# Performance work log

Hardware: AMD Instinct MI355X
Metric: run time of the kernel (lower is better)

## Reference

```python
import jax, jax.numpy as jnp
import numpy as np

N_NODES = 50000
N_EDGES = 800000
D_IN = 128
H1 = 128
H2 = 64
N_CLASSES = 4


def _sage_conv(x, src, dst, w_l, w_r, b, num_nodes):
    # PyG SAGEConv (aggr='mean'): out = lin_l(mean_{j->i} x_j) + lin_r(x_i)
    ones = jnp.ones((src.shape[0],), dtype=x.dtype)
    deg = jax.ops.segment_sum(ones, dst, num_segments=num_nodes)  # [N]
    agg = jax.ops.segment_sum(x[src], dst, num_segments=num_nodes)  # [N, d]
    agg = agg / jnp.maximum(deg, 1.0)[:, None]
    return agg @ w_l + b + x @ w_r


def setup_inputs() -> dict:
    key = jax.random.key(0)
    ks = jax.random.split(key, 12)
    x_content = jax.random.normal(ks[0], (N_NODES, D_IN), dtype=jnp.float32)
    edge_index = jax.random.randint(ks[1], (2, N_EDGES), 0, N_NODES, dtype=jnp.int32)
    edge_type = jax.random.randint(ks[2], (N_EDGES,), 0, 4, dtype=jnp.int32)
    s = 0.05
    params = {
        'w_l0': jax.random.normal(ks[3], (D_IN, H1), jnp.float32) * s,
        'w_r0': jax.random.normal(ks[4], (D_IN, H1), jnp.float32) * s,
        'b0': jnp.zeros((H1,), jnp.float32),
        'w_l1': jax.random.normal(ks[5], (H1, H1), jnp.float32) * s,
        'w_r1': jax.random.normal(ks[6], (H1, H1), jnp.float32) * s,
        'b1': jnp.zeros((H1,), jnp.float32),
        'w_l2': jax.random.normal(ks[7], (H1, H2), jnp.float32) * s,
        'w_r2': jax.random.normal(ks[8], (H1, H2), jnp.float32) * s,
        'b2': jnp.zeros((H2,), jnp.float32),
        'w_out': jax.random.normal(ks[9], (H2, N_CLASSES), jnp.float32) * s,
        'b_out': jnp.zeros((N_CLASSES,), jnp.float32),
    }
    return {'x_content': x_content, 'edge_index': edge_index, 'edge_type': edge_type, **params}


def reference(x_content, edge_index, edge_type,
              w_l0, w_r0, b0, w_l1, w_r1, b1, w_l2, w_r2, b2, w_out, b_out):
    # eval mode: dropout is identity
    src, dst = edge_index[0], edge_index[1]
    n = x_content.shape[0]
    x = x_content
    for (wl, wr, b) in ((w_l0, w_r0, b0), (w_l1, w_r1, b1), (w_l2, w_r2, b2)):
        x = _sage_conv(x, src, dst, wl, wr, b, n)
        x = jax.nn.relu(x)
    return x @ w_out + b_out
```

## Files before the change

kernel.cpp:

```cpp
#include <hip/hip_runtime.h>
#include <hip/hip_fp16.h>

#define D 128

constexpr int RSH = 14;
constexpr int RSZ = 1 << RSH;
constexpr int NRANGE = 4;
constexpr int CSH = 15;
constexpr int CSZ = 1 << CSH;

using short8 = __attribute__((ext_vector_type(8))) short;
using f32x4 = __attribute__((ext_vector_type(4))) float;

__device__ inline void splitf(float v, unsigned short& h, unsigned short& l) {
    unsigned b = __float_as_uint(v);
    h = (unsigned short)(b >> 16);
    float fh = __uint_as_float(b & 0xffff0000u);
    float r = v - fh;
    l = (unsigned short)(__float_as_uint(r) >> 16);
}

struct WSplitArgs {
    const float* src[6];
    unsigned short* dh[6];
    unsigned short* dl[6];
    int n[6];
};

__global__ __launch_bounds__(256) void split_w(WSplitArgs a) {
    int m = blockIdx.y;
    int N = a.n[m];
    int e = blockIdx.x * 256 + threadIdx.x;
    if (e >= 128 * N) return;
    int sh = (N == 128) ? 7 : 6;
    int k = e >> sh;
    int n = e & (N - 1);
    float v = a.src[m][e];
    unsigned short h, l;
    splitf(v, h, l);
    a.dh[m][n * 128 + k] = h;
    a.dl[m][n * 128 + k] = l;
}

__global__ __launch_bounds__(1024) void hist_gemm_x(
    const int* __restrict__ dst, unsigned* __restrict__ hist,
    unsigned short* __restrict__ rank, int n_edges, int nchunk, int nhist,
    const float* __restrict__ X,
    const unsigned short* __restrict__ W1h, const unsigned short* __restrict__ W1l,
    const unsigned short* __restrict__ W2h, const unsigned short* __restrict__ W2l,
    const float* __restrict__ bias, __half* __restrict__ P, float* __restrict__ Q, int M) {
    __shared__ __align__(16) char smem[2 * 16 * 65 * 16];

    const int b = blockIdx.x;
    const int tid = threadIdx.x;

    if (b < nhist) {
        unsigned* lh = (unsigned*)smem;
        int r = b & (NRANGE - 1), c = b >> 2;
        for (int i = tid; i < RSZ / 2; i += 1024) lh[i] = 0;
        __syncthreads();
        int e0 = c << CSH, e1 = min(n_edges, e0 + CSZ);
        for (int e = e0 + tid; e < e1; e += 1024) {
            int d = dst[e];
            if ((d >> RSH) == r) {
                int ii = d & (RSZ - 1);
                unsigned sh = (ii & 1) * 16;
                unsigned old = atomicAdd(&lh[ii >> 1], 1u << sh);
                rank[e] = (unsigned short)((old >> sh) & 0xffffu);
            }
        }
        __syncthreads();
        unsigned* gh = hist + (size_t)(r * nchunk + c) * (RSZ / 2);
        for (int i = tid; i < RSZ / 2; i += 1024) gh[i] = lh[i];
        return;
    }

    short8(*As)[16 * 65] = (short8(*)[16 * 65])smem;
    const int wave = tid >> 6;
    const int lane = tid & 63;
    const int l15 = lane & 15;
    const int q = lane >> 4;
    const int m0 = (b - nhist) * 64;

    {
        int row = tid >> 4, col16 = tid & 15;
        int gr = min(m0 + row, M - 1);
        const float4* xp = (const float4*)X + (size_t)gr * 32 + col16 * 2;
        float4 v0 = xp[0], v1 = xp[1];
        float fv[8] = {v0.x, v0.y, v0.z, v0.w, v1.x, v1.y, v1.z, v1.w};
        short8 h, l;
#pragma unroll
        for (int j = 0; j < 8; ++j) {
            unsigned short hh_, ll_;
            splitf(fv[j], hh_, ll_);
            h[j] = (short)hh_;
            l[j] = (short)ll_;
        }
        As[0][col16 * 65 + row] = h;
        As[1][col16 * 65 + row] = l;
    }
    __syncthreads();

    const int isQ = wave >> 3;
    const int colbase = (wave & 7) * 16;
    const unsigned short* Wh = isQ ? W2h : W1h;
    const unsigned short* Wl = isQ ? W2l : W1l;
    const float bv = isQ ? bias[colbase + l15] : 0.f;
    const int wbase = (colbase + l15) * 128 + q * 8;

    f32x4 acc[4] = {};
    short8 Bh = *(const short8*)(Wh + wbase);
    short8 Bl = *(const short8*)(Wl + wbase);

#pragma unroll 1
    for (int kt = 0; kt < 4; ++kt) {
        short8 nBh, nBl;
        if (kt < 3) {
            nBh = *(const short8*)(Wh + wbase + (kt + 1) * 32);
            nBl = *(const short8*)(Wl + wbase + (kt + 1) * 32);
        }
#pragma unroll
        for (int mt = 0; mt < 4; ++mt) {
            int ai = (kt * 4 + q) * 65 + mt * 16 + l15;
            short8 Afh = As[0][ai];
            short8 Afl = As[1][ai];
            acc[mt] = __builtin_amdgcn_mfma_f32_16x16x32_bf16(Afh, Bh, acc[mt], 0, 0, 0);
            acc[mt] = __builtin_amdgcn_mfma_f32_16x16x32_bf16(Afh, Bl, acc[mt], 0, 0, 0);
            acc[mt] = __builtin_amdgcn_mfma_f32_16x16x32_bf16(Afl, Bh, acc[mt], 0, 0, 0);
        }
        Bh = nBh; Bl = nBl;
    }

    const int col = colbase + l15;
#pragma unroll
    for (int mt = 0; mt < 4; ++mt) {
        int orow = m0 + mt * 16 + q * 4;
#pragma unroll
        for (int r = 0; r < 4; ++r) {
            int rr = orow + r;
            if (rr < M) {
                if (isQ) Q[(size_t)rr * 128 + col] = acc[mt][r] + bv;
                else P[(size_t)rr * 128 + col] = __float2half(acc[mt][r]);
            }
        }
    }
}

__global__ __launch_bounds__(256) void deg_sum_partials(
    const unsigned short* __restrict__ hist16, int* __restrict__ deg,
    int* __restrict__ partials, int n_nodes, int nchunk) {
    __shared__ int sd[256];
    int b = blockIdx.x, t = threadIdx.x;
    int i = b * 256 + t;
    int s = 0;
    if (i < n_nodes) {
        int r = i >> RSH, ii = i & (RSZ - 1);
        const unsigned short* hp = hist16 + (size_t)r * nchunk * RSZ + ii;
        for (int c = 0; c < nchunk; ++c) s += hp[(size_t)c * RSZ];
        deg[i] = s;
    }
    sd[t] = s;
    __syncthreads();
    for (int st = 128; st > 0; st >>= 1) {
        if (t < st) sd[t] += sd[t + st];
        __syncthreads();
    }
    if (t == 0) partials[b] = sd[0];
}

__global__ __launch_bounds__(256) void scan_fill(
    const int* __restrict__ deg, const int* __restrict__ partials,
    const unsigned short* __restrict__ hist16, int* __restrict__ row_ptr,
    float* __restrict__ inv_deg, int* __restrict__ base,
    int n_nodes, int nchunk, int nblk) {
    __shared__ int sp[256];
    __shared__ int sd[256];
    int b = blockIdx.x, t = threadIdx.x;

    sp[t] = (t < b && t < nblk) ? partials[t] : 0;
    __syncthreads();
    for (int st = 128; st > 0; st >>= 1) {
        if (t < st) sp[t] += sp[t + st];
        __syncthreads();
    }
    int pbase = sp[0];

    int i = b * 256 + t;
    int v = (i < n_nodes) ? deg[i] : 0;
    sd[t] = v;
    __syncthreads();
    for (int d = 1; d < 256; d <<= 1) {
        int x = (t >= d) ? sd[t - d] : 0;
        __syncthreads();
        sd[t] += x;
        __syncthreads();
    }
    int excl = sd[t] - v + pbase;
    if (i < n_nodes) {
        row_ptr[i] = excl;
        int dv = v > 1 ? v : 1;
        inv_deg[i] = 1.0f / (float)dv;
        if (i == n_nodes - 1) row_ptr[n_nodes] = excl + v;
        int r = i >> RSH, ii = i & (RSZ - 1);
        int bacc = excl;
        for (int c = 0; c < nchunk; ++c) {
            size_t idx = (size_t)(r * nchunk + c) * RSZ + ii;
            base[idx] = bacc;
            bacc += hist16[idx];
        }
    }
}

__global__ __launch_bounds__(256) void fill_edges(
    const int* __restrict__ src, const int* __restrict__ dst,
    const unsigned short* __restrict__ rank, const int* __restrict__ base,
    int* __restrict__ csr, int n_edges, int nchunk) {
    int e = blockIdx.x * 256 + threadIdx.x;
    if (e >= n_edges) return;
    int d = dst[e];
    int c = e >> CSH;
    int r = d >> RSH;
    int slot = base[(size_t)(r * nchunk + c) * RSZ + (d & (RSZ - 1))] + rank[e];
    csr[slot] = src[e];
}

template <int BN>
__global__ __launch_bounds__(2 * (BN / 16) * 64) void gemm_wide(
    const unsigned short* __restrict__ Ah, const unsigned short* __restrict__ Al,
    const unsigned short* __restrict__ W1h, const unsigned short* __restrict__ W1l,
    const unsigned short* __restrict__ W2h, const unsigned short* __restrict__ W2l,
    const float* __restrict__ bias, __half* __restrict__ P, float* __restrict__ Q, int M) {
    __shared__ short8 As[2][16 * 65];
    constexpr int NW = BN / 16;
    constexpr int NTH = 2 * NW * 64;

    const int tid = threadIdx.x;
    const int wave = tid >> 6;
    const int lane = tid & 63;
    const int l15 = lane & 15;
    const int q = lane >> 4;
    const int m0 = blockIdx.x * 64;

#pragma unroll
    for (int it = 0; it < 2048 / NTH; ++it) {
        int s = it * NTH + tid;
        int arr = s >> 10;
        int sp = s & 1023;
        int row = sp >> 4, col16 = sp & 15;
        int gr = min(m0 + row, M - 1);
        const unsigned short* src = (arr ? Al : Ah) + (size_t)gr * 128 + col16 * 8;
        As[arr][col16 * 65 + row] = *(const short8*)src;
    }
    __syncthreads();

    const int isQ = wave >= NW;
    const int colbase = (isQ ? (wave - NW) : wave) * 16;
    const unsigned short* Wh = isQ ? W2h : W1h;
    const unsigned short* Wl = isQ ? W2l : W1l;
    const float bv = isQ ? bias[colbase + l15] : 0.f;
    const int wbase = (colbase + l15) * 128 + q * 8;

    f32x4 acc[4] = {};
    short8 Bh = *(const short8*)(Wh + wbase);
    short8 Bl = *(const short8*)(Wl + wbase);

#pragma unroll 1
    for (int kt = 0; kt < 4; ++kt) {
        short8 nBh, nBl;
        if (kt < 3) {
            nBh = *(const short8*)(Wh + wbase + (kt + 1) * 32);
            nBl = *(const short8*)(Wl + wbase + (kt + 1) * 32);
        }
#pragma unroll
        for (int mt = 0; mt < 4; ++mt) {
            int ai = (kt * 4 + q) * 65 + mt * 16 + l15;
            short8 Afh = As[0][ai];
            short8 Afl = As[1][ai];
            acc[mt] = __builtin_amdgcn_mfma_f32_16x16x32_bf16(Afh, Bh, acc[mt], 0, 0, 0);
            acc[mt] = __builtin_amdgcn_mfma_f32_16x16x32_bf16(Afh, Bl, acc[mt], 0, 0, 0);
            acc[mt] = __builtin_amdgcn_mfma_f32_16x16x32_bf16(Afl, Bh, acc[mt], 0, 0, 0);
        }
        Bh = nBh; Bl = nBl;
    }

    const int col = colbase + l15;
#pragma unroll
    for (int mt = 0; mt < 4; ++mt) {
        int orow = m0 + mt * 16 + q * 4;
#pragma unroll
        for (int r = 0; r < 4; ++r) {
            int rr = orow + r;
            if (rr < M) {
                if (isQ) Q[(size_t)rr * BN + col] = acc[mt][r] + bv;
                else P[(size_t)rr * BN + col] = __float2half(acc[mt][r]);
            }
        }
    }
}

__global__ __launch_bounds__(256) void agg_fused128(
    const __half* __restrict__ P, const float* __restrict__ Q,
    const int* __restrict__ row_ptr, const int* __restrict__ csr,
    const float* __restrict__ inv_deg, unsigned short* __restrict__ Hh,
    unsigned short* __restrict__ Hl, int n_nodes) {
    int node = (blockIdx.x * blockDim.x + threadIdx.x) >> 6;
    int lane = threadIdx.x & 63;
    if (node >= n_nodes) return;
    int beg = row_ptr[node], end = row_ptr[node + 1];
    const int g = lane >> 4;
    const int l = lane & 15;
    float a[4][8] = {};
    int e = beg;
    bool have = (e + 16 <= end);
    int i0 = 0, i1 = 0, i2 = 0, i3 = 0;
    if (have) { i0 = csr[e + g]; i1 = csr[e + 4 + g]; i2 = csr[e + 8 + g]; i3 = csr[e + 12 + g]; }
    while (have) {
        int en = e + 16;
        bool hn = (en + 16 <= end);
        int n0 = 0, n1 = 0, n2 = 0, n3 = 0;
        if (hn) { n0 = csr[en + g]; n1 = csr[en + 4 + g]; n2 = csr[en + 8 + g]; n3 = csr[en + 12 + g]; }
        int ss[4] = {i0, i1, i2, i3};
#pragma unroll
        for (int j = 0; j < 4; ++j) {
            uint4 raw = *(const uint4*)(P + (size_t)ss[j] * 128 + l * 8);
            float2 f01 = __half22float2(*reinterpret_cast<__half2*>(&raw.x));
            float2 f23 = __half22float2(*reinterpret_cast<__half2*>(&raw.y));
            float2 f45 = __half22float2(*reinterpret_cast<__half2*>(&raw.z));
            float2 f67 = __half22float2(*reinterpret_cast<__half2*>(&raw.w));
            a[j][0] += f01.x; a[j][1] += f01.y; a[j][2] += f23.x; a[j][3] += f23.y;
            a[j][4] += f45.x; a[j][5] += f45.y; a[j][6] += f67.x; a[j][7] += f67.y;
        }
        e = en; i0 = n0; i1 = n1; i2 = n2; i3 = n3; have = hn;
    }
    if (e < end) {
        int p0 = e + g, p1 = e + 4 + g, p2 = e + 8 + g, p3 = e + 12 + g;
        int j0 = (p0 < end) ? csr[p0] : -1;
        int j1 = (p1 < end) ? csr[p1] : -1;
        int j2 = (p2 < end) ? csr[p2] : -1;
        int j3 = (p3 < end) ? csr[p3] : -1;
        int ss[4] = {j0, j1, j2, j3};
#pragma unroll
        for (int j = 0; j < 4; ++j) {
            if (ss[j] >= 0) {
                uint4 raw = *(const uint4*)(P + (size_t)ss[j] * 128 + l * 8);
                float2 f01 = __half22float2(*reinterpret_cast<__half2*>(&raw.x));
                float2 f23 = __half22float2(*reinterpret_cast<__half2*>(&raw.y));
                float2 f45 = __half22float2(*reinterpret_cast<__half2*>(&raw.z));
                float2 f67 = __half22float2(*reinterpret_cast<__half2*>(&raw.w));
                a[j][0] += f01.x; a[j][1] += f01.y; a[j][2] += f23.x; a[j][3] += f23.y;
                a[j][4] += f45.x; a[j][5] += f45.y; a[j][6] += f67.x; a[j][7] += f67.y;
            }
        }
    }
    float s[8];
#pragma unroll
    for (int k = 0; k < 8; ++k) {
        s[k] = (a[0][k] + a[1][k]) + (a[2][k] + a[3][k]);
        s[k] += __shfl_xor(s[k], 16);
        s[k] += __shfl_xor(s[k], 32);
    }
    if (lane < 16) {
        float w = inv_deg[node];
        const float4* Q4 = (const float4*)Q;
        float4 q0 = Q4[(size_t)node * 32 + 2 * l];
        float4 q1 = Q4[(size_t)node * 32 + 2 * l + 1];
        float h0 = fmaxf(fmaf(s[0], w, q0.x), 0.f);
        float h1 = fmaxf(fmaf(s[1], w, q0.y), 0.f);
        float h2 = fmaxf(fmaf(s[2], w, q0.z), 0.f);
        float h3 = fmaxf(fmaf(s[3], w, q0.w), 0.f);
        float h4 = fmaxf(fmaf(s[4], w, q1.x), 0.f);
        float h5 = fmaxf(fmaf(s[5], w, q1.y), 0.f);
        float h6 = fmaxf(fmaf(s[6], w, q1.z), 0.f);
        float h7 = fmaxf(fmaf(s[7], w, q1.w), 0.f);
        ushort4 hv0, lv0, hv1, lv1;
        splitf(h0, hv0.x, lv0.x);
        splitf(h1, hv0.y, lv0.y);
        splitf(h2, hv0.z, lv0.z);
        splitf(h3, hv0.w, lv0.w);
        splitf(h4, hv1.x, lv1.x);
        splitf(h5, hv1.y, lv1.y);
        splitf(h6, hv1.z, lv1.z);
        splitf(h7, hv1.w, lv1.w);
        ((ushort4*)Hh)[(size_t)node * 32 + 2 * l] = hv0;
        ((ushort4*)Hh)[(size_t)node * 32 + 2 * l + 1] = hv1;
        ((ushort4*)Hl)[(size_t)node * 32 + 2 * l] = lv0;
        ((ushort4*)Hl)[(size_t)node * 32 + 2 * l + 1] = lv1;
    }
}

__global__ __launch_bounds__(256) void agg64_head(
    const __half* __restrict__ P, const float* __restrict__ Q,
    const int* __restrict__ row_ptr, const int* __restrict__ csr,
    const float* __restrict__ inv_deg, const float* __restrict__ Wo,
    const float* __restrict__ bo, float* __restrict__ out, int n_nodes) {
    int node = (blockIdx.x * blockDim.x + threadIdx.x) >> 6;
    int lane = threadIdx.x & 63;
    if (node >= n_nodes) return;
    int beg = row_ptr[node], end = row_ptr[node + 1];
    const int g = lane >> 4;
    const int l = lane & 15;
    float a[4][4] = {};
    int e = beg;
    bool have = (e + 16 <= end);
    int i0 = 0, i1 = 0, i2 = 0, i3 = 0;
    if (have) { i0 = csr[e + g]; i1 = csr[e + 4 + g]; i2 = csr[e + 8 + g]; i3 = csr[e + 12 + g]; }
    while (have) {
        int en = e + 16;
        bool hn = (en + 16 <= end);
        int n0 = 0, n1 = 0, n2 = 0, n3 = 0;
        if (hn) { n0 = csr[en + g]; n1 = csr[en + 4 + g]; n2 = csr[en + 8 + g]; n3 = csr[en + 12 + g]; }
        int ss[4] = {i0, i1, i2, i3};
#pragma unroll
        for (int j = 0; j < 4; ++j) {
            uint2 raw = *(const uint2*)(P + (size_t)ss[j] * 64 + l * 4);
            float2 f01 = __half22float2(*reinterpret_cast<__half2*>(&raw.x));
            float2 f23 = __half22float2(*reinterpret_cast<__half2*>(&raw.y));
            a[j][0] += f01.x; a[j][1] += f01.y; a[j][2] += f23.x; a[j][3] += f23.y;
        }
        e = en; i0 = n0; i1 = n1; i2 = n2; i3 = n3; have = hn;
    }
    if (e < end) {
        int p0 = e + g, p1 = e + 4 + g, p2 = e + 8 + g, p3 = e + 12 + g;
        int j0 = (p0 < end) ? csr[p0] : -1;
        int j1 = (p1 < end) ? csr[p1] : -1;
        int j2 = (p2 < end) ? csr[p2] : -1;
        int j3 = (p3 < end) ? csr[p3] : -1;
        int ss[4] = {j0, j1, j2, j3};
#pragma unroll
        for (int j = 0; j < 4; ++j) {
            if (ss[j] >= 0) {
                uint2 raw = *(const uint2*)(P + (size_t)ss[j] * 64 + l * 4);
                float2 f01 = __half22float2(*reinterpret_cast<__half2*>(&raw.x));
                float2 f23 = __half22float2(*reinterpret_cast<__half2*>(&raw.y));
                a[j][0] += f01.x; a[j][1] += f01.y; a[j][2] += f23.x; a[j][3] += f23.y;
            }
        }
    }
    float s0 = (a[0][0] + a[1][0]) + (a[2][0] + a[3][0]);
    float s1 = (a[0][1] + a[1][1]) + (a[2][1] + a[3][1]);
    float s2 = (a[0][2] + a[1][2]) + (a[2][2] + a[3][2]);
    float s3 = (a[0][3] + a[1][3]) + (a[2][3] + a[3][3]);
    s0 += __shfl_xor(s0, 16); s0 += __shfl_xor(s0, 32);
    s1 += __shfl_xor(s1, 16); s1 += __shfl_xor(s1, 32);
    s2 += __shfl_xor(s2, 16); s2 += __shfl_xor(s2, 32);
    s3 += __shfl_xor(s3, 16); s3 += __shfl_xor(s3, 32);
    if (lane < 16) {
        float w = inv_deg[node];
        float4 qv = ((const float4*)Q)[(size_t)node * 16 + l];
        float h0 = fmaxf(fmaf(s0, w, qv.x), 0.f);
        float h1 = fmaxf(fmaf(s1, w, qv.y), 0.f);
        float h2 = fmaxf(fmaf(s2, w, qv.z), 0.f);
        float h3 = fmaxf(fmaf(s3, w, qv.w), 0.f);
        const float4* Wo4 = (const float4*)Wo;
        float4 w0 = Wo4[4 * l + 0], w1 = Wo4[4 * l + 1], w2 = Wo4[4 * l + 2], w3 = Wo4[4 * l + 3];
        float c0 = h0 * w0.x + h1 * w1.x + h2 * w2.x + h3 * w3.x;
        float c1 = h0 * w0.y + h1 * w1.y + h2 * w2.y + h3 * w3.y;
        float c2 = h0 * w0.z + h1 * w1.z + h2 * w2.z + h3 * w3.z;
        float c3 = h0 * w0.w + h1 * w1.w + h2 * w2.w + h3 * w3.w;
#pragma unroll
        for (int m = 8; m > 0; m >>= 1) {
            c0 += __shfl_xor(c0, m);
            c1 += __shfl_xor(c1, m);
            c2 += __shfl_xor(c2, m);
            c3 += __shfl_xor(c3, m);
        }
        if (l == 0) {
            float4 r;
            r.x = c0 + bo[0];
            r.y = c1 + bo[1];
            r.z = c2 + bo[2];
            r.w = c3 + bo[3];
            ((float4*)out)[node] = r;
        }
    }
}

extern "C" void kernel_launch(void* const* d_in, const int* in_sizes, int n_in,
                              void* d_out, int out_size, void* d_ws, size_t ws_size,
                              hipStream_t stream) {
    const float* x = (const float*)d_in[0];
    const int* ei = (const int*)d_in[1];
    const float* wl0 = (const float*)d_in[3];
    const float* wr0 = (const float*)d_in[4];
    const float* b0 = (const float*)d_in[5];
    const float* wl1 = (const float*)d_in[6];
    const float* wr1 = (const float*)d_in[7];
    const float* b1 = (const float*)d_in[8];
    const float* wl2 = (const float*)d_in[9];
    const float* wr2 = (const float*)d_in[10];
    const float* b2 = (const float*)d_in[11];
    const float* wo = (const float*)d_in[12];
    const float* bo = (const float*)d_in[13];

    const int n_nodes = in_sizes[0] / D;
    const int n_edges = in_sizes[1] / 2;
    const int* srcp = ei;
    const int* dstp = ei + n_edges;

    char* ws = (char*)d_ws;
    size_t off = 0;
    auto carve = [&](size_t bytes) -> void* {
        void* p = ws + off;
        off = (off + bytes + 255) & ~(size_t)255;
        return p;
    };
    int* deg = (int*)carve((size_t)n_nodes * 4);
    int* row_ptr = (int*)carve((size_t)(n_nodes + 1) * 4);
    int* partials = (int*)carve(256 * 4);
    float* inv_deg = (float*)carve((size_t)n_nodes * 4);
    unsigned short* rankb = (unsigned short*)carve((size_t)n_edges * 2);
    int* csr = (int*)carve((size_t)n_edges * 4);
    __half* Pbuf = (__half*)carve((size_t)n_nodes * D * 2);
    float* Qbuf = (float*)carve((size_t)n_nodes * D * 4);
    unsigned short* hh = (unsigned short*)carve((size_t)n_nodes * D * 2);
    unsigned short* hl = (unsigned short*)carve((size_t)n_nodes * D * 2);
    unsigned short* wt = (unsigned short*)carve((size_t)(4 * 128 * 128 + 2 * 64 * 128) * 2 * 2);
    unsigned short* wl0h = wt;
    unsigned short* wl0l = wl0h + 128 * 128;
    unsigned short* wr0h = wl0l + 128 * 128;
    unsigned short* wr0l = wr0h + 128 * 128;
    unsigned short* wl1h = wr0l + 128 * 128;
    unsigned short* wl1l = wl1h + 128 * 128;
    unsigned short* wr1h = wl1l + 128 * 128;
    unsigned short* wr1l = wr1h + 128 * 128;
    unsigned short* wl2h = wr1l + 128 * 128;
    unsigned short* wl2l = wl2h + 64 * 128;
    unsigned short* wr2h = wl2l + 64 * 128;
    unsigned short* wr2l = wr2h + 64 * 128;

    const int nchunk = (n_edges + CSZ - 1) >> CSH;
    unsigned* hist = (unsigned*)carve((size_t)NRANGE * nchunk * (RSZ / 2) * 4);
    unsigned short* hist16 = (unsigned short*)hist;
    int* basep = (int*)carve((size_t)NRANGE * nchunk * RSZ * 4);

    const int nblk = (n_nodes + 255) / 256;
    const int nhist = NRANGE * nchunk;
    const int gemm_blocks = (n_nodes + 63) / 64;
    const int agg_blocks = (n_nodes * 64 + 255) / 256;

    WSplitArgs wa;
    wa.src[0] = wl0; wa.dh[0] = wl0h; wa.dl[0] = wl0l; wa.n[0] = 128;
    wa.src[1] = wr0; wa.dh[1] = wr0h; wa.dl[1] = wr0l; wa.n[1] = 128;
    wa.src[2] = wl1; wa.dh[2] = wl1h; wa.dl[2] = wl1l; wa.n[2] = 128;
    wa.src[3] = wr1; wa.dh[3] = wr1h; wa.dl[3] = wr1l; wa.n[3] = 128;
    wa.src[4] = wl2; wa.dh[4] = wl2h; wa.dl[4] = wl2l; wa.n[4] = 64;
    wa.src[5] = wr2; wa.dh[5] = wr2h; wa.dl[5] = wr2l; wa.n[5] = 64;

    split_w<<<dim3(64, 6), 256, 0, stream>>>(wa);
    hist_gemm_x<<<nhist + gemm_blocks, 1024, 0, stream>>>(
        dstp, hist, rankb, n_edges, nchunk, nhist,
        x, wl0h, wl0l, wr0h, wr0l, b0, Pbuf, Qbuf, n_nodes);
    deg_sum_partials<<<nblk, 256, 0, stream>>>(hist16, deg, partials, n_nodes, nchunk);
    scan_fill<<<nblk, 256, 0, stream>>>(deg, partials, hist16, row_ptr, inv_deg, basep,
                                        n_nodes, nchunk, nblk);
    fill_edges<<<(n_edges + 255) / 256, 256, 0, stream>>>(srcp, dstp, rankb, basep, csr,
                                                          n_edges, nchunk);
    agg_fused128<<<agg_blocks, 256, 0, stream>>>(Pbuf, Qbuf, row_ptr, csr, inv_deg, hh, hl, n_nodes);
    gemm_wide<128><<<gemm_blocks, 1024, 0, stream>>>(
        hh, hl, wl1h, wl1l, wr1h, wr1l, b1, Pbuf, Qbuf, n_nodes);
    agg_fused128<<<agg_blocks, 256, 0, stream>>>(Pbuf, Qbuf, row_ptr, csr, inv_deg, hh, hl, n_nodes);
    gemm_wide<64><<<gemm_blocks, 512, 0, stream>>>(
        hh, hl, wl2h, wl2l, wr2h, wr2l, b2, Pbuf, Qbuf, n_nodes);
    agg64_head<<<agg_blocks, 256, 0, stream>>>(Pbuf, Qbuf, row_ptr, csr, inv_deg,
                                               wo, bo, (float*)d_out, n_nodes);
}
```

Measured before the change: 293.9 us.

## Spread layer-0 GEMM tiles across CSR build kernels to fill idle CUs

The layer-0 input GEMM tiles, previously all launched alongside the histogram blocks, are now split across the histogram, degree-sum, scan and fill kernels. Each of these CSR-construction kernels gets some GEMM tiles appended so the light, low-occupancy phases overlap with tensor work. The degree, scan and fill kernels also move from 256 to 1024 threads per block, which shrinks their grids (the scan's partials prefix handles up to 1024 blocks). The tile counts are hardcoded at 250 per stage, and each kernel now reserves GEMM-sized shared memory, which may reduce occupancy of the small CSR blocks.

```diff
diff --git a/kernel.cpp b/kernel.cpp
--- a/kernel.cpp
+++ b/kernel.cpp
@@ -42,19 +42,95 @@
     a.dl[m][n * 128 + k] = l;
 }
 
-__global__ __launch_bounds__(1024) void hist_gemm_x(
+__device__ __forceinline__ void gemm_x_tile(
+    char* smem, int tile, const float* __restrict__ X,
+    const unsigned short* __restrict__ W1h, const unsigned short* __restrict__ W1l,
+    const unsigned short* __restrict__ W2h, const unsigned short* __restrict__ W2l,
+    const float* __restrict__ bias, __half* __restrict__ P, float* __restrict__ Q, int M) {
+    short8(*As)[16 * 65] = (short8(*)[16 * 65])smem;
+    const int tid = threadIdx.x;
+    const int wave = tid >> 6;
+    const int lane = tid & 63;
+    const int l15 = lane & 15;
+    const int q = lane >> 4;
+    const int m0 = tile * 64;
+
+    {
+        int row = tid >> 4, col16 = tid & 15;
+        int gr = min(m0 + row, M - 1);
+        const float4* xp = (const float4*)X + (size_t)gr * 32 + col16 * 2;
+        float4 v0 = xp[0], v1 = xp[1];
+        float fv[8] = {v0.x, v0.y, v0.z, v0.w, v1.x, v1.y, v1.z, v1.w};
+        short8 h, l;
+#pragma unroll
+        for (int j = 0; j < 8; ++j) {
+            unsigned short hh_, ll_;
+            splitf(fv[j], hh_, ll_);
+            h[j] = (short)hh_;
+            l[j] = (short)ll_;
+        }
+        As[0][col16 * 65 + row] = h;
+        As[1][col16 * 65 + row] = l;
+    }
+    __syncthreads();
+
+    const int isQ = wave >> 3;
+    const int colbase = (wave & 7) * 16;
+    const unsigned short* Wh = isQ ? W2h : W1h;
+    const unsigned short* Wl = isQ ? W2l : W1l;
+    const float bv = isQ ? bias[colbase + l15] : 0.f;
+    const int wbase = (colbase + l15) * 128 + q * 8;
+
+    f32x4 acc[4] = {};
+    short8 Bh = *(const short8*)(Wh + wbase);
+    short8 Bl = *(const short8*)(Wl + wbase);
+
+#pragma unroll 1
+    for (int kt = 0; kt < 4; ++kt) {
+        short8 nBh, nBl;
+        if (kt < 3) {
+            nBh = *(const short8*)(Wh + wbase + (kt + 1) * 32);
+            nBl = *(const short8*)(Wl + wbase + (kt + 1) * 32);
+        }
+#pragma unroll
+        for (int mt = 0; mt < 4; ++mt) {
+            int ai = (kt * 4 + q) * 65 + mt * 16 + l15;
+            short8 Afh = As[0][ai];
+            short8 Afl = As[1][ai];
+            acc[mt] = __builtin_amdgcn_mfma_f32_16x16x32_bf16(Afh, Bh, acc[mt], 0, 0, 0);
+            acc[mt] = __builtin_amdgcn_mfma_f32_16x16x32_bf16(Afh, Bl, acc[mt], 0, 0, 0);
+            acc[mt] = __builtin_amdgcn_mfma_f32_16x16x32_bf16(Afl, Bh, acc[mt], 0, 0, 0);
+        }
+        Bh = nBh; Bl = nBl;
+    }
+
+    const int col = colbase + l15;
+#pragma unroll
+    for (int mt = 0; mt < 4; ++mt) {
+        int orow = m0 + mt * 16 + q * 4;
+#pragma unroll
+        for (int r = 0; r < 4; ++r) {
+            int rr = orow + r;
+            if (rr < M) {
+                if (isQ) Q[(size_t)rr * 128 + col] = acc[mt][r] + bv;
+                else P[(size_t)rr * 128 + col] = __float2half(acc[mt][r]);
+            }
+        }
+    }
+}
+
+__global__ __launch_bounds__(1024) void hist_gemm(
     const int* __restrict__ dst, unsigned* __restrict__ hist,
-    unsigned short* __restrict__ rank, int n_edges, int nchunk, int nhist,
+    unsigned short* __restrict__ rank, int n_edges, int nchunk, int ncsr, int tbase,
     const float* __restrict__ X,
     const unsigned short* __restrict__ W1h, const unsigned short* __restrict__ W1l,
     const unsigned short* __restrict__ W2h, const unsigned short* __restrict__ W2l,
     const float* __restrict__ bias, __half* __restrict__ P, float* __restrict__ Q, int M) {
     __shared__ __align__(16) char smem[2 * 16 * 65 * 16];
-
     const int b = blockIdx.x;
     const int tid = threadIdx.x;
 
-    if (b < nhist) {
+    if (b < ncsr) {
         unsigned* lh = (unsigned*)smem;
         int r = b & (NRANGE - 1), c = b >> 2;
         for (int i = tid; i < RSZ / 2; i += 1024) lh[i] = 0;
@@ -74,154 +150,120 @@
         for (int i = tid; i < RSZ / 2; i += 1024) gh[i] = lh[i];
         return;
     }
-
-    short8(*As)[16 * 65] = (short8(*)[16 * 65])smem;
-    const int wave = tid >> 6;
-    const int lane = tid & 63;
-    const int l15 = lane & 15;
-    const int q = lane >> 4;
-    const int m0 = (b - nhist) * 64;
-
-    {
-        int row = tid >> 4, col16 = tid & 15;
-        int gr = min(m0 + row, M - 1);
-        const float4* xp = (const float4*)X + (size_t)gr * 32 + col16 * 2;
-        float4 v0 = xp[0], v1 = xp[1];
-        float fv[8] = {v0.x, v0.y, v0.z, v0.w, v1.x, v1.y, v1.z, v1.w};
-        short8 h, l;
-#pragma unroll
-        for (int j = 0; j < 8; ++j) {
-            unsigned short hh_, ll_;
-            splitf(fv[j], hh_, ll_);
-            h[j] = (short)hh_;
-            l[j] = (short)ll_;
-        }
-        As[0][col16 * 65 + row] = h;
-        As[1][col16 * 65 + row] = l;
-    }
-    __syncthreads();
-
-    const int isQ = wave >> 3;
-    const int colbase = (wave & 7) * 16;
-    const unsigned short* Wh = isQ ? W2h : W1h;
-    const unsigned short* Wl = isQ ? W2l : W1l;
-    const float bv = isQ ? bias[colbase + l15] : 0.f;
-    const int wbase = (colbase + l15) * 128 + q * 8;
-
-    f32x4 acc[4] = {};
-    short8 Bh = *(const short8*)(Wh + wbase);
-    short8 Bl = *(const short8*)(Wl + wbase);
-
-#pragma unroll 1
-    for (int kt = 0; kt < 4; ++kt) {
-        short8 nBh, nBl;
-        if (kt < 3) {
-            nBh = *(const short8*)(Wh + wbase + (kt + 1) * 32);
-            nBl = *(const short8*)(Wl + wbase + (kt + 1) * 32);
-        }
-#pragma unroll
-        for (int mt = 0; mt < 4; ++mt) {
-            int ai = (kt * 4 + q) * 65 + mt * 16 + l15;
-            short8 Afh = As[0][ai];
-            short8 Afl = As[1][ai];
-            acc[mt] = __builtin_amdgcn_mfma_f32_16x16x32_bf16(Afh, Bh, acc[mt], 0, 0, 0);
-            acc[mt] = __builtin_amdgcn_mfma_f32_16x16x32_bf16(Afh, Bl, acc[mt], 0, 0, 0);
-            acc[mt] = __builtin_amdgcn_mfma_f32_16x16x32_bf16(Afl, Bh, acc[mt], 0, 0, 0);
-        }
-        Bh = nBh; Bl = nBl;
-    }
-
-    const int col = colbase + l15;
-#pragma unroll
-    for (int mt = 0; mt < 4; ++mt) {
-        int orow = m0 + mt * 16 + q * 4;
-#pragma unroll
-        for (int r = 0; r < 4; ++r) {
-            int rr = orow + r;
-            if (rr < M) {
-                if (isQ) Q[(size_t)rr * 128 + col] = acc[mt][r] + bv;
-                else P[(size_t)rr * 128 + col] = __float2half(acc[mt][r]);
-            }
-        }
-    }
-}
-
-__global__ __launch_bounds__(256) void deg_sum_partials(
+    gemm_x_tile(smem, tbase + b - ncsr, X, W1h, W1l, W2h, W2l, bias, P, Q, M);
+}
+
+__global__ __launch_bounds__(1024) void deg_gemm(
     const unsigned short* __restrict__ hist16, int* __restrict__ deg,
-    int* __restrict__ partials, int n_nodes, int nchunk) {
-    __shared__ int sd[256];
-    int b = blockIdx.x, t = threadIdx.x;
-    int i = b * 256 + t;
-    int s = 0;
-    if (i < n_nodes) {
-        int r = i >> RSH, ii = i & (RSZ - 1);
-        const unsigned short* hp = hist16 + (size_t)r * nchunk * RSZ + ii;
-        for (int c = 0; c < nchunk; ++c) s += hp[(size_t)c * RSZ];
-        deg[i] = s;
-    }
-    sd[t] = s;
-    __syncthreads();
-    for (int st = 128; st > 0; st >>= 1) {
-        if (t < st) sd[t] += sd[t + st];
+    int* __restrict__ partials, int n_nodes, int nchunk, int ncsr, int tbase,
+    const float* __restrict__ X,
+    const unsigned short* __restrict__ W1h, const unsigned short* __restrict__ W1l,
+    const unsigned short* __restrict__ W2h, const unsigned short* __restrict__ W2l,
+    const float* __restrict__ bias, __half* __restrict__ P, float* __restrict__ Q, int M) {
+    __shared__ __align__(16) char smem[2 * 16 * 65 * 16];
+    const int b = blockIdx.x;
+    const int t = threadIdx.x;
+
+    if (b < ncsr) {
+        int* sd = (int*)smem;
+        int i = b * 1024 + t;
+        int s = 0;
+        if (i < n_nodes) {
+            int r = i >> RSH, ii = i & (RSZ - 1);
+            const unsigned short* hp = hist16 + (size_t)r * nchunk * RSZ + ii;
+            for (int c = 0; c < nchunk; ++c) s += hp[(size_t)c * RSZ];
+            deg[i] = s;
+        }
+        sd[t] = s;
         __syncthreads();
-    }
-    if (t == 0) partials[b] = sd[0];
-}
-
-__global__ __launch_bounds__(256) void scan_fill(
+        for (int st = 512; st > 0; st >>= 1) {
+            if (t < st) sd[t] += sd[t + st];
+            __syncthreads();
+        }
+        if (t == 0) partials[b] = sd[0];
+        return;
+    }
+    gemm_x_tile(smem, tbase + b - ncsr, X, W1h, W1l, W2h, W2l, bias, P, Q, M);
+}
+
+__global__ __launch_bounds__(1024) void scan_gemm(
     const int* __restrict__ deg, const int* __restrict__ partials,
     const unsigned short* __restrict__ hist16, int* __restrict__ row_ptr,
     float* __restrict__ inv_deg, int* __restrict__ base,
-    int n_nodes, int nchunk, int nblk) {
-    __shared__ int sp[256];
-    __shared__ int sd[256];
-    int b = blockIdx.x, t = threadIdx.x;
-
-    sp[t] = (t < b && t < nblk) ? partials[t] : 0;
-    __syncthreads();
-    for (int st = 128; st > 0; st >>= 1) {
-        if (t < st) sp[t] += sp[t + st];
+    int n_nodes, int nchunk, int nblk, int ncsr, int tbase,
+    const float* __restrict__ X,
+    const unsigned short* __restrict__ W1h, const unsigned short* __restrict__ W1l,
+    const unsigned short* __restrict__ W2h, const unsigned short* __restrict__ W2l,
+    const float* __restrict__ bias, __half* __restrict__ P, float* __restrict__ Q, int M) {
+    __shared__ __align__(16) char smem[2 * 16 * 65 * 16];
+    const int b = blockIdx.x;
+    const int t = threadIdx.x;
+
+    if (b < ncsr) {
+        int* sp = (int*)smem;
+        int* sd = sp + 1024;
+
+        sp[t] = (t < b && t < nblk) ? partials[t] : 0;
         __syncthreads();
-    }
-    int pbase = sp[0];
-
-    int i = b * 256 + t;
-    int v = (i < n_nodes) ? deg[i] : 0;
-    sd[t] = v;
-    __syncthreads();
-    for (int d = 1; d < 256; d <<= 1) {
-        int x = (t >= d) ? sd[t - d] : 0;
+        for (int st = 512; st > 0; st >>= 1) {
+            if (t < st) sp[t] += sp[t + st];
+            __syncthreads();
+        }
+        int pbase = sp[0];
+
+        int i = b * 1024 + t;
+        int v = (i < n_nodes) ? deg[i] : 0;
+        sd[t] = v;
         __syncthreads();
-        sd[t] += x;
-        __syncthreads();
-    }
-    int excl = sd[t] - v + pbase;
-    if (i < n_nodes) {
-        row_ptr[i] = excl;
-        int dv = v > 1 ? v : 1;
-        inv_deg[i] = 1.0f / (float)dv;
-        if (i == n_nodes - 1) row_ptr[n_nodes] = excl + v;
-        int r = i >> RSH, ii = i & (RSZ - 1);
-        int bacc = excl;
-        for (int c = 0; c < nchunk; ++c) {
-            size_t idx = (size_t)(r * nchunk + c) * RSZ + ii;
-            base[idx] = bacc;
-            bacc += hist16[idx];
-        }
-    }
-}
-
-__global__ __launch_bounds__(256) void fill_edges(
+        for (int d = 1; d < 1024; d <<= 1) {
+            int x = (t >= d) ? sd[t - d] : 0;
+            __syncthreads();
+            sd[t] += x;
+            __syncthreads();
+        }
+        int excl = sd[t] - v + pbase;
+        if (i < n_nodes) {
+            row_ptr[i] = excl;
+            int dv = v > 1 ? v : 1;
+            inv_deg[i] = 1.0f / (float)dv;
+            if (i == n_nodes - 1) row_ptr[n_nodes] = excl + v;
+            int r = i >> RSH, ii = i & (RSZ - 1);
+            int bacc = excl;
+            for (int c = 0; c < nchunk; ++c) {
+                size_t idx = (size_t)(r * nchunk + c) * RSZ + ii;
+                base[idx] = bacc;
+                bacc += hist16[idx];
+            }
+        }
+        return;
+    }
+    gemm_x_tile(smem, tbase + b - ncsr, X, W1h, W1l, W2h, W2l, bias, P, Q, M);
+}
+
+__global__ __launch_bounds__(1024) void fill_gemm(
     const int* __restrict__ src, const int* __restrict__ dst,
     const unsigned short* __restrict__ rank, const int* __restrict__ base,
-    int* __restrict__ csr, int n_edges, int nchunk) {
-    int e = blockIdx.x * 256 + threadIdx.x;
-    if (e >= n_edges) return;
-    int d = dst[e];
-    int c = e >> CSH;
-    int r = d >> RSH;
-    int slot = base[(size_t)(r * nchunk + c) * RSZ + (d & (RSZ - 1))] + rank[e];
-    csr[slot] = src[e];
+    int* __restrict__ csr, int n_edges, int nchunk, int ncsr, int tbase,
+    const float* __restrict__ X,
+    const unsigned short* __restrict__ W1h, const unsigned short* __restrict__ W1l,
+    const unsigned short* __restrict__ W2h, const unsigned short* __restrict__ W2l,
+    const float* __restrict__ bias, __half* __restrict__ P, float* __restrict__ Q, int M) {
+    __shared__ __align__(16) char smem[2 * 16 * 65 * 16];
+    const int b = blockIdx.x;
+    const int t = threadIdx.x;
+
+    if (b < ncsr) {
+        int e = b * 1024 + t;
+        if (e < n_edges) {
+            int d = dst[e];
+            int c = e >> CSH;
+            int r = d >> RSH;
+            int slot = base[(size_t)(r * nchunk + c) * RSZ + (d & (RSZ - 1))] + rank[e];
+            csr[slot] = src[e];
+        }
+        return;
+    }
+    gemm_x_tile(smem, tbase + b - ncsr, X, W1h, W1l, W2h, W2l, bias, P, Q, M);
 }
 
 template <int BN>
@@ -533,10 +575,14 @@
     unsigned short* hist16 = (unsigned short*)hist;
     int* basep = (int*)carve((size_t)NRANGE * nchunk * RSZ * 4);
 
-    const int nblk = (n_nodes + 255) / 256;
     const int nhist = NRANGE * nchunk;
+    const int ndeg = (n_nodes + 1023) / 1024;
+    const int nfill = (n_edges + 1023) / 1024;
     const int gemm_blocks = (n_nodes + 63) / 64;
     const int agg_blocks = (n_nodes * 64 + 255) / 256;
+
+    const int t1 = 250, t2 = 250, t3 = 250;
+    const int t4 = gemm_blocks - t1 - t2 - t3;
 
     WSplitArgs wa;
     wa.src[0] = wl0; wa.dh[0] = wl0h; wa.dl[0] = wl0l; wa.n[0] = 128;
@@ -547,14 +593,19 @@
     wa.src[5] = wr2; wa.dh[5] = wr2h; wa.dl[5] = wr2l; wa.n[5] = 64;
 
     split_w<<<dim3(64, 6), 256, 0, stream>>>(wa);
-    hist_gemm_x<<<nhist + gemm_blocks, 1024, 0, stream>>>(
-        dstp, hist, rankb, n_edges, nchunk, nhist,
+    hist_gemm<<<nhist + t1, 1024, 0, stream>>>(
+        dstp, hist, rankb, n_edges, nchunk, nhist, 0,
         x, wl0h, wl0l, wr0h, wr0l, b0, Pbuf, Qbuf, n_nodes);
-    deg_sum_partials<<<nblk, 256, 0, stream>>>(hist16, deg, partials, n_nodes, nchunk);
-    scan_fill<<<nblk, 256, 0, stream>>>(deg, partials, hist16, row_ptr, inv_deg, basep,
-                                        n_nodes, nchunk, nblk);
-    fill_edges<<<(n_edges + 255) / 256, 256, 0, stream>>>(srcp, dstp, rankb, basep, csr,
-                                                          n_edges, nchunk);
+    deg_gemm<<<ndeg + t2, 1024, 0, stream>>>(
+        hist16, deg, partials, n_nodes, nchunk, ndeg, t1,
+        x, wl0h, wl0l, wr0h, wr0l, b0, Pbuf, Qbuf, n_nodes);
+    scan_gemm<<<ndeg + t3, 1024, 0, stream>>>(
+        deg, partials, hist16, row_ptr, inv_deg, basep, n_nodes, nchunk, ndeg,
+        ndeg, t1 + t2,
+        x, wl0h, wl0l, wr0h, wr0l, b0, Pbuf, Qbuf, n_nodes);
+    fill_gemm<<<nfill + t4, 1024, 0, stream>>>(
+        srcp, dstp, rankb, basep, csr, n_edges, nchunk, nfill, t1 + t2 + t3,
+        x, wl0h, wl0l, wr0h, wr0l, b0, Pbuf, Qbuf, n_nodes);
     agg_fused128<<<agg_blocks, 256, 0, stream>>>(Pbuf, Qbuf, row_ptr, csr, inv_deg, hh, hl, n_nodes);
     gemm_wide<128><<<gemm_blocks, 1024, 0, stream>>>(
         hh, hl, wl1h, wl1l, wr1h, wr1l, b1, Pbuf, Qbuf, n_nodes);
```

After: 303.6 us. 1.03x slower.
